# Kernel optimization log

Hardware: AMD Instinct MI355X
Metric: run time of the kernel (lower is better)

## Reference

```python
import jax, jax.numpy as jnp
import numpy as np

# Model dims (match init_kwargs)
D_MODEL = 512
NUM_EXPERTS = 8
TOP_K = 2
FFN_MULT = 2
HIDDEN = FFN_MULT * D_MODEL
BATCH, SEQ = 4, 2048


def setup_inputs() -> dict:
    key = jax.random.key(0)
    k_x, k_g, k_bg, k_w1, k_w3, k_w2 = jax.random.split(key, 6)
    sd = 1.0 / np.sqrt(D_MODEL).astype(np.float32)
    sh = 1.0 / np.sqrt(HIDDEN).astype(np.float32)
    return {
        "x": jax.random.normal(k_x, (BATCH, SEQ, D_MODEL), dtype=jnp.float32),
        # gate: nn.Linear(d_model, num_experts) with bias
        "Wg": jax.random.normal(k_g, (D_MODEL, NUM_EXPERTS), dtype=jnp.float32) * sd,
        "bg": jax.random.normal(k_bg, (NUM_EXPERTS,), dtype=jnp.float32) * 0.01,
        # stacked per-expert SwiGLU FFN params (no bias, LLaMA-style)
        "W1": jax.random.normal(k_w1, (NUM_EXPERTS, D_MODEL, HIDDEN), dtype=jnp.float32) * sd,
        "W3": jax.random.normal(k_w3, (NUM_EXPERTS, D_MODEL, HIDDEN), dtype=jnp.float32) * sd,
        "W2": jax.random.normal(k_w2, (NUM_EXPERTS, HIDDEN, D_MODEL), dtype=jnp.float32) * sh,
    }


def reference(x, Wg, bg, W1, W3, W2):
    B, S, D = x.shape
    E = Wg.shape[1]
    xt = x.reshape(-1, D)                        # [T, D], T = B*S
    T = xt.shape[0]

    # Router: top-k over experts, softmax over the k selected logits
    logits = xt @ Wg + bg                        # [T, E]
    top_vals, top_idx = jax.lax.top_k(logits, TOP_K)  # [T, K]
    top_probs = jax.nn.softmax(top_vals, axis=-1)     # [T, K]

    # Dense per-(token, expert) combine weight; zero where expert not selected.
    # top-k indices are distinct per token so scatter-add == scatter-set.
    gate_w = jnp.zeros((T, E), dtype=xt.dtype).at[
        jnp.arange(T)[:, None], top_idx
    ].add(top_probs)                              # [T, E]

    # Loop over experts (fixed, small), accumulate weighted expert outputs.
    def body(y, expert):
        w1, w3, w2, g = expert                   # g: [T]
        h = jax.nn.silu(xt @ w1) * (xt @ w3)     # [T, H]
        return y + g[:, None] * (h @ w2), None

    y0 = jnp.zeros_like(xt)
    y, _ = jax.lax.scan(body, y0, (W1, W3, W2, gate_w.T))
    return y.reshape(B, S, D)
```

## Files before the change

kernel.cpp:

```cpp
#include <hip/hip_runtime.h>
#include <hip/hip_bf16.h>

#define TOKENS 8192
#define DM 512
#define NE 8
#define HID 1024
#define NSLOT (TOKENS * 2)
#define NB 32

#define BM 128
#define BN 64
#define BK 64
#define BN2 128
#define MAXTILE 136

typedef __bf16 bf16x8 __attribute__((ext_vector_type(8)));
typedef float floatx4 __attribute__((ext_vector_type(4)));
typedef unsigned short u16x8 __attribute__((ext_vector_type(8)));

__device__ __forceinline__ unsigned short f2bf(float f) {
    union { float f; unsigned u; } c; c.f = f;
    unsigned u = c.u;
    u += 0x7fffu + ((u >> 16) & 1u);
    return (unsigned short)(u >> 16);
}

__device__ __forceinline__ void load16_lds(const void* g, void* l) {
    __builtin_amdgcn_global_load_lds(
        (const __attribute__((address_space(1))) unsigned int*)g,
        (__attribute__((address_space(3))) unsigned int*)l, 16, 0, 0);
}

__global__ void cvt_transpose_kernel(const float* __restrict__ W1, const float* __restrict__ W3,
                                     const float* __restrict__ W2,
                                     unsigned short* __restrict__ w1t, unsigned short* __restrict__ w3t,
                                     unsigned short* __restrict__ w2t) {
    __shared__ float tile[64][65];
    const float* src; unsigned short* dst; int K, N;
    if (blockIdx.y == 0)      { src = W1; dst = w1t; K = DM;  N = HID; }
    else if (blockIdx.y == 1) { src = W3; dst = w3t; K = DM;  N = HID; }
    else                      { src = W2; dst = w2t; K = HID; N = DM;  }
    const int tkn = (K >> 6) * (N >> 6);
    int b = blockIdx.x;
    int e = b / tkn;
    int rem = b % tkn;
    const int tn6 = N >> 6;
    int kt = rem / tn6, nt = rem % tn6;
    int tx = threadIdx.x & 15, ty = threadIdx.x >> 4;
    const float* s = src + ((size_t)(e * K + kt * 64 + ty)) * N + nt * 64 + tx * 4;
    #pragma unroll
    for (int i = 0; i < 4; i++) {
        float4 v = *(const float4*)(s + (size_t)(i * 16) * N);
        float* tr = &tile[ty + i * 16][tx * 4];
        tr[0] = v.x; tr[1] = v.y; tr[2] = v.z; tr[3] = v.w;
    }
    __syncthreads();
    int n = threadIdx.x >> 3;
    int c8 = (threadIdx.x & 7) * 8;
    unsigned short* d = dst + ((size_t)(e * N + nt * 64)) * K + kt * 64;
    #pragma unroll
    for (int i = 0; i < 2; i++) {
        int nn = n + i * 32;
        u16x8 r;
        #pragma unroll
        for (int kk = 0; kk < 8; kk++) r[kk] = f2bf(tile[c8 + kk][nn]);
        *(u16x8*)(d + (size_t)nn * K + c8) = r;
    }
}

__global__ void router_kernel(const float* __restrict__ x, const float* __restrict__ Wg,
                              const float* __restrict__ bg,
                              int* __restrict__ top_idx, float* __restrict__ top_p,
                              unsigned short* __restrict__ xb) {
    int lane = threadIdx.x & 63, wave = threadIdx.x >> 6;
    int t = blockIdx.x * 4 + wave;
    float acc[NE];
    #pragma unroll
    for (int e = 0; e < NE; e++) acc[e] = 0.f;
    const float* xr = x + (size_t)t * DM;
    unsigned short* xbr = xb + (size_t)t * DM;
    #pragma unroll
    for (int j = 0; j < 8; j++) {
        int d = lane + j * 64;
        float xv = xr[d];
        xbr[d] = f2bf(xv);
        const float4* wr = (const float4*)(Wg + (size_t)d * NE);
        float4 w0 = wr[0], w1 = wr[1];
        acc[0] += xv * w0.x; acc[1] += xv * w0.y; acc[2] += xv * w0.z; acc[3] += xv * w0.w;
        acc[4] += xv * w1.x; acc[5] += xv * w1.y; acc[6] += xv * w1.z; acc[7] += xv * w1.w;
    }
    #pragma unroll
    for (int e = 0; e < NE; e++) {
        float v = acc[e];
        #pragma unroll
        for (int off = 32; off > 0; off >>= 1) v += __shfl_down(v, off, 64);
        acc[e] = v;
    }
    if (lane == 0) {
        float best = -1e30f, second = -1e30f;
        int bi = 0, si = 0;
        #pragma unroll
        for (int e = 0; e < NE; e++) {
            float v = acc[e] + bg[e];
            if (v > best) { second = best; si = bi; best = v; bi = e; }
            else if (v > second) { second = v; si = e; }
        }
        float ex = __expf(second - best);
        float inv = 1.f / (1.f + ex);
        top_idx[t * 2] = bi;  top_idx[t * 2 + 1] = si;
        top_p[t * 2] = inv;   top_p[t * 2 + 1] = ex * inv;
    }
}

__global__ void hist_kernel(const int* __restrict__ top_idx, int* __restrict__ block_hist) {
    __shared__ int h[NE];
    int b = blockIdx.x, tid = threadIdx.x;
    if (tid < NE) h[tid] = 0;
    __syncthreads();
    int t = b * 256 + tid;
    atomicAdd(&h[top_idx[t * 2]], 1);
    atomicAdd(&h[top_idx[t * 2 + 1]], 1);
    __syncthreads();
    if (tid < NE) block_hist[b * NE + tid] = h[tid];
}

__global__ void prefix_kernel(const int* __restrict__ block_hist, int* __restrict__ counts,
                              int* __restrict__ offsets, int* __restrict__ bases) {
    int e = threadIdx.x;
    if (e < NE) {
        int run = 0;
        for (int b = 0; b < NB; b++) { bases[b * NE + e] = run; run += block_hist[b * NE + e]; }
        counts[e] = run;
    }
    __syncthreads();
    if (e == 0) {
        int s = 0;
        for (int ee = 0; ee < NE; ee++) { offsets[ee] = s; s += counts[ee]; }
    }
    __syncthreads();
    if (e < NE) {
        int off = offsets[e];
        for (int b = 0; b < NB; b++) bases[b * NE + e] += off;
    }
}

__global__ void build_kernel(const int* __restrict__ top_idx, const float* __restrict__ top_p,
                             const int* __restrict__ bases,
                             int* __restrict__ rows, float* __restrict__ gates,
                             int* __restrict__ slot_of) {
    __shared__ int cur[NE];
    int b = blockIdx.x, tid = threadIdx.x;
    if (tid < NE) cur[tid] = bases[b * NE + tid];
    __syncthreads();
    int t = b * 256 + tid;
    #pragma unroll
    for (int k = 0; k < 2; k++) {
        int e = top_idx[t * 2 + k];
        int slot = atomicAdd(&cur[e], 1);
        rows[slot] = t;
        gates[slot] = top_p[t * 2 + k];
        slot_of[t * 2 + k] = slot;
    }
}

__device__ __forceinline__ bool tile_lookup(const int* counts, const int* offsets, int gy,
                                            int& e, int& mt, int& cnt, int& off) {
    int bacc = 0;
    #pragma unroll
    for (int ee = 0; ee < NE; ee++) {
        int c = counts[ee];
        int ntl = (c + BM - 1) >> 7;
        if (gy < bacc + ntl) { e = ee; mt = gy - bacc; cnt = c; off = offsets[ee]; return true; }
        bacc += ntl;
    }
    return false;
}

__global__ __launch_bounds__(256) void gemm1_kernel(
    const unsigned short* __restrict__ xb,
    const unsigned short* __restrict__ w1t,
    const unsigned short* __restrict__ w3t,
    unsigned short* __restrict__ Hb,
    const int* __restrict__ rows, const int* __restrict__ counts,
    const int* __restrict__ offsets) {
    const int lid = blockIdx.x;
    const int xcd = lid & 7;
    const int j = lid >> 3;
    const int gy = xcd * (MAXTILE / 8) + (j >> 4);
    const int nt = j & 15;
    int e, mt, cnt, off;
    if (!tile_lookup(counts, offsets, gy, e, mt, cnt, off)) return;

    __shared__ unsigned short As[BM * BK];
    __shared__ unsigned short B1s[BN * BK];
    __shared__ unsigned short B3s[BN * BK];

    const int tid = threadIdx.x;
    const int lane = tid & 63, wave = tid >> 6;
    const int lrow8 = lane >> 3;
    const int lchunk = (lane & 7) ^ lrow8;

    const unsigned short* a_g[4];
    #pragma unroll
    for (int i = 0; i < 4; i++) {
        int r = (wave * 4 + i) * 8 + lrow8;
        int gr = mt * BM + r;
        int tok = rows[off + (gr < cnt ? gr : 0)];
        a_g[i] = xb + (size_t)tok * DM + lchunk * 8;
    }
    const unsigned short* b1_g[2]; const unsigned short* b3_g[2];
    #pragma unroll
    for (int i = 0; i < 2; i++) {
        int r = (wave * 2 + i) * 8 + lrow8;
        b1_g[i] = w1t + ((size_t)e * HID + nt * BN + r) * DM + lchunk * 8;
        b3_g[i] = w3t + ((size_t)e * HID + nt * BN + r) * DM + lchunk * 8;
    }

    const int l15 = lane & 15, quad = lane >> 4;
    const int sw = l15 & 7;

    floatx4 acc1[2][4], acc3[2][4];
    #pragma unroll
    for (int i = 0; i < 2; i++)
        #pragma unroll
        for (int j2 = 0; j2 < 4; j2++) {
            acc1[i][j2] = (floatx4){0.f, 0.f, 0.f, 0.f};
            acc3[i][j2] = (floatx4){0.f, 0.f, 0.f, 0.f};
        }

    auto stage = [&](int k0) {
        #pragma unroll
        for (int i = 0; i < 4; i++) load16_lds(a_g[i] + k0, &As[(wave * 4 + i) * 512]);
        #pragma unroll
        for (int i = 0; i < 2; i++) {
            load16_lds(b1_g[i] + k0, &B1s[(wave * 2 + i) * 512]);
            load16_lds(b3_g[i] + k0, &B3s[(wave * 2 + i) * 512]);
        }
    };
    auto compute = [&]() {
        #pragma unroll
        for (int kk = 0; kk < 2; kk++) {
            const int qc = kk * 4 + quad;
            const int ch = (qc ^ sw) << 3;
            bf16x8 af[2], b1f[4], b3f[4];
            #pragma unroll
            for (int mi = 0; mi < 2; mi++)
                af[mi] = *(const bf16x8*)(&As[(wave * 32 + mi * 16 + l15) * 64 + ch]);
            #pragma unroll
            for (int ni = 0; ni < 4; ni++) {
                b1f[ni] = *(const bf16x8*)(&B1s[(ni * 16 + l15) * 64 + ch]);
                b3f[ni] = *(const bf16x8*)(&B3s[(ni * 16 + l15) * 64 + ch]);
            }
            #pragma unroll
            for (int mi = 0; mi < 2; mi++)
                #pragma unroll
                for (int ni = 0; ni < 4; ni++) {
                    acc1[mi][ni] = __builtin_amdgcn_mfma_f32_16x16x32_bf16(af[mi], b1f[ni], acc1[mi][ni], 0, 0, 0);
                    acc3[mi][ni] = __builtin_amdgcn_mfma_f32_16x16x32_bf16(af[mi], b3f[ni], acc3[mi][ni], 0, 0, 0);
                }
        }
    };

    const int NI = DM / BK;
    #pragma unroll
    for (int i = 0; i < NI; i++) {
        if (i) __syncthreads();
        stage(i * BK);
        __syncthreads();
        compute();
    }
    #pragma unroll
    for (int mi = 0; mi < 2; mi++) {
        #pragma unroll
        for (int r = 0; r < 4; r++) {
            int mloc = wave * 32 + mi * 16 + quad * 4 + r;
            int gi = mt * BM + mloc;
            if (gi < cnt) {
                size_t rowbase = (size_t)(off + gi) * HID + nt * BN;
                #pragma unroll
                for (int ni = 0; ni < 4; ni++) {
                    float z1 = acc1[mi][ni][r];
                    float z3 = acc3[mi][ni][r];
                    float h = (z1 / (1.f + __expf(-z1))) * z3;
                    Hb[rowbase + ni * 16 + l15] = f2bf(h);
                }
            }
        }
    }
}

__global__ __launch_bounds__(256) void gemm2_kernel(
    const unsigned short* __restrict__ Hb,
    const unsigned short* __restrict__ w2t,
    unsigned short* __restrict__ P,
    const float* __restrict__ gates,
    const int* __restrict__ counts, const int* __restrict__ offsets) {
    const int lid = blockIdx.x;
    const int xcd = lid & 7;
    const int j = lid >> 3;
    const int gy = xcd * (MAXTILE / 8) + (j >> 2);
    const int nt = j & 3;
    int e, mt, cnt, off;
    if (!tile_lookup(counts, offsets, gy, e, mt, cnt, off)) return;

    __shared__ unsigned short As[BM * BK];
    __shared__ unsigned short Bs[BN2 * BK];

    const int tid = threadIdx.x;
    const int lane = tid & 63, wave = tid >> 6;
    const int lrow8 = lane >> 3;
    const int lchunk = (lane & 7) ^ lrow8;

    const unsigned short* a_g[4];
    #pragma unroll
    for (int i = 0; i < 4; i++) {
        int r = (wave * 4 + i) * 8 + lrow8;
        int sl = off + mt * BM + r;
        if (sl >= NSLOT) sl = NSLOT - 1;
        a_g[i] = Hb + (size_t)sl * HID + lchunk * 8;
    }
    const unsigned short* b_g[4];
    #pragma unroll
    for (int i = 0; i < 4; i++) {
        int r = (wave * 4 + i) * 8 + lrow8;
        b_g[i] = w2t + ((size_t)e * DM + nt * BN2 + r) * HID + lchunk * 8;
    }

    const int l15 = lane & 15, quad = lane >> 4;
    const int sw = l15 & 7;

    floatx4 acc[2][8];
    #pragma unroll
    for (int i = 0; i < 2; i++)
        #pragma unroll
        for (int j2 = 0; j2 < 8; j2++) acc[i][j2] = (floatx4){0.f, 0.f, 0.f, 0.f};

    auto stage = [&](int k0) {
        #pragma unroll
        for (int i = 0; i < 4; i++) load16_lds(a_g[i] + k0, &As[(wave * 4 + i) * 512]);
        #pragma unroll
        for (int i = 0; i < 4; i++) load16_lds(b_g[i] + k0, &Bs[(wave * 4 + i) * 512]);
    };
    auto compute = [&]() {
        #pragma unroll
        for (int kk = 0; kk < 2; kk++) {
            const int qc = kk * 4 + quad;
            const int ch = (qc ^ sw) << 3;
            bf16x8 af[2], bf[8];
            #pragma unroll
            for (int mi = 0; mi < 2; mi++)
                af[mi] = *(const bf16x8*)(&As[(wave * 32 + mi * 16 + l15) * 64 + ch]);
            #pragma unroll
            for (int ni = 0; ni < 8; ni++)
                bf[ni] = *(const bf16x8*)(&Bs[(ni * 16 + l15) * 64 + ch]);
            #pragma unroll
            for (int mi = 0; mi < 2; mi++)
                #pragma unroll
                for (int ni = 0; ni < 8; ni++)
                    acc[mi][ni] = __builtin_amdgcn_mfma_f32_16x16x32_bf16(af[mi], bf[ni], acc[mi][ni], 0, 0, 0);
        }
    };

    const int NI = HID / BK;
    #pragma unroll
    for (int i = 0; i < NI; i++) {
        if (i) __syncthreads();
        stage(i * BK);
        __syncthreads();
        compute();
    }
    #pragma unroll
    for (int mi = 0; mi < 2; mi++) {
        #pragma unroll
        for (int r = 0; r < 4; r++) {
            int mloc = wave * 32 + mi * 16 + quad * 4 + r;
            int gi = mt * BM + mloc;
            if (gi < cnt) {
                int slot = off + gi;
                float g = gates[slot];
                #pragma unroll
                for (int ni = 0; ni < 8; ni++) {
                    int col = nt * BN2 + ni * 16 + l15;
                    P[(size_t)slot * DM + col] = f2bf(g * acc[mi][ni][r]);
                }
            }
        }
    }
}

__global__ void combine_kernel(const unsigned short* __restrict__ P,
                               const int* __restrict__ slot_of, float* __restrict__ y) {
    int i = blockIdx.x * blockDim.x + threadIdx.x;
    int t = i / (DM / 8);
    int c8 = i % (DM / 8);
    int s0 = slot_of[t * 2], s1 = slot_of[t * 2 + 1];
    uint4 a = *(const uint4*)(P + (size_t)s0 * DM + c8 * 8);
    uint4 b = *(const uint4*)(P + (size_t)s1 * DM + c8 * 8);
    float o[8];
    const unsigned* aw = (const unsigned*)&a;
    const unsigned* bw = (const unsigned*)&b;
    #pragma unroll
    for (int j = 0; j < 4; j++) {
        union { unsigned u; float f; } al, ah, bl, bh;
        al.u = aw[j] << 16; ah.u = aw[j] & 0xffff0000u;
        bl.u = bw[j] << 16; bh.u = bw[j] & 0xffff0000u;
        o[j * 2]     = al.f + bl.f;
        o[j * 2 + 1] = ah.f + bh.f;
    }
    float4* yo = (float4*)(y + (size_t)t * DM + c8 * 8);
    yo[0] = make_float4(o[0], o[1], o[2], o[3]);
    yo[1] = make_float4(o[4], o[5], o[6], o[7]);
}

extern "C" void kernel_launch(void* const* d_in, const int* in_sizes, int n_in,
                              void* d_out, int out_size, void* d_ws, size_t ws_size,
                              hipStream_t stream) {
    (void)in_sizes; (void)n_in; (void)out_size; (void)ws_size;
    const float* x  = (const float*)d_in[0];
    const float* Wg = (const float*)d_in[1];
    const float* bg = (const float*)d_in[2];
    const float* W1 = (const float*)d_in[3];
    const float* W3 = (const float*)d_in[4];
    const float* W2 = (const float*)d_in[5];
    float* y = (float*)d_out;

    char* p = (char*)d_ws;
    auto carve = [&](size_t bytes) -> char* {
        char* r = p;
        p += (bytes + 255) & ~(size_t)255;
        return r;
    };
    unsigned short* xb   = (unsigned short*)carve((size_t)TOKENS * DM * 2);
    unsigned short* w1t  = (unsigned short*)carve((size_t)NE * DM * HID * 2);
    unsigned short* w3t  = (unsigned short*)carve((size_t)NE * DM * HID * 2);
    unsigned short* w2t  = (unsigned short*)carve((size_t)NE * HID * DM * 2);
    unsigned short* Hb   = (unsigned short*)carve((size_t)NSLOT * HID * 2);
    int*   rows    = (int*)carve(NSLOT * 4);
    float* gates   = (float*)carve(NSLOT * 4);
    int*   slot_of = (int*)carve(NSLOT * 4);
    int*   tidx    = (int*)carve((size_t)TOKENS * 2 * 4);
    float* tp      = (float*)carve((size_t)TOKENS * 2 * 4);
    int*   counts  = (int*)carve(256);
    int*   offsets = (int*)carve(256);
    int*   bhist   = (int*)carve((size_t)NB * NE * 4);
    int*   bases   = (int*)carve((size_t)NB * NE * 4);
    unsigned short* P = w1t;

    router_kernel<<<dim3(TOKENS / 4), dim3(256), 0, stream>>>(x, Wg, bg, tidx, tp, xb);
    cvt_transpose_kernel<<<dim3(NE * 8 * 16, 3), dim3(256), 0, stream>>>(W1, W3, W2, w1t, w3t, w2t);
    hist_kernel<<<dim3(NB), dim3(256), 0, stream>>>(tidx, bhist);
    prefix_kernel<<<dim3(1), dim3(64), 0, stream>>>(bhist, counts, offsets, bases);
    build_kernel<<<dim3(NB), dim3(256), 0, stream>>>(tidx, tp, bases, rows, gates, slot_of);
    gemm1_kernel<<<dim3((HID / BN) * MAXTILE), dim3(256), 0, stream>>>(xb, w1t, w3t, Hb, rows, counts, offsets);
    gemm2_kernel<<<dim3((DM / BN2) * MAXTILE), dim3(256), 0, stream>>>(Hb, w2t, P, gates, counts, offsets);
    combine_kernel<<<dim3((TOKENS * DM / 8) / 256), dim3(256), 0, stream>>>(P, slot_of, y);
}
```

Baseline: 199.5 us.

## Fuse router with weight conversion, split-K gemm2 with atomic scatter into output

Merges the router and weight convert/transpose kernels into one launch. gemm2 now splits the hidden dimension in two and atomically adds gated results straight into y, which removes the bf16 P buffer and the combine kernel. y is zeroed with a memset beforehand. This doubles the gemm2 grid for more parallelism but adds four fp32 atomics per output element (two K halves times two experts) and makes the summation order nondeterministic.

```diff
diff --git a/kernel.cpp b/kernel.cpp
--- a/kernel.cpp
+++ b/kernel.cpp
@@ -31,84 +31,87 @@
         (__attribute__((address_space(3))) unsigned int*)l, 16, 0, 0);
 }
 
-__global__ void cvt_transpose_kernel(const float* __restrict__ W1, const float* __restrict__ W3,
-                                     const float* __restrict__ W2,
-                                     unsigned short* __restrict__ w1t, unsigned short* __restrict__ w3t,
-                                     unsigned short* __restrict__ w2t) {
-    __shared__ float tile[64][65];
-    const float* src; unsigned short* dst; int K, N;
-    if (blockIdx.y == 0)      { src = W1; dst = w1t; K = DM;  N = HID; }
-    else if (blockIdx.y == 1) { src = W3; dst = w3t; K = DM;  N = HID; }
-    else                      { src = W2; dst = w2t; K = HID; N = DM;  }
-    const int tkn = (K >> 6) * (N >> 6);
-    int b = blockIdx.x;
-    int e = b / tkn;
-    int rem = b % tkn;
-    const int tn6 = N >> 6;
-    int kt = rem / tn6, nt = rem % tn6;
-    int tx = threadIdx.x & 15, ty = threadIdx.x >> 4;
-    const float* s = src + ((size_t)(e * K + kt * 64 + ty)) * N + nt * 64 + tx * 4;
-    #pragma unroll
-    for (int i = 0; i < 4; i++) {
-        float4 v = *(const float4*)(s + (size_t)(i * 16) * N);
-        float* tr = &tile[ty + i * 16][tx * 4];
-        tr[0] = v.x; tr[1] = v.y; tr[2] = v.z; tr[3] = v.w;
-    }
-    __syncthreads();
-    int n = threadIdx.x >> 3;
-    int c8 = (threadIdx.x & 7) * 8;
-    unsigned short* d = dst + ((size_t)(e * N + nt * 64)) * K + kt * 64;
-    #pragma unroll
-    for (int i = 0; i < 2; i++) {
-        int nn = n + i * 32;
-        u16x8 r;
-        #pragma unroll
-        for (int kk = 0; kk < 8; kk++) r[kk] = f2bf(tile[c8 + kk][nn]);
-        *(u16x8*)(d + (size_t)nn * K + c8) = r;
-    }
-}
-
-__global__ void router_kernel(const float* __restrict__ x, const float* __restrict__ Wg,
-                              const float* __restrict__ bg,
-                              int* __restrict__ top_idx, float* __restrict__ top_p,
-                              unsigned short* __restrict__ xb) {
-    int lane = threadIdx.x & 63, wave = threadIdx.x >> 6;
-    int t = blockIdx.x * 4 + wave;
-    float acc[NE];
-    #pragma unroll
-    for (int e = 0; e < NE; e++) acc[e] = 0.f;
-    const float* xr = x + (size_t)t * DM;
-    unsigned short* xbr = xb + (size_t)t * DM;
-    #pragma unroll
-    for (int j = 0; j < 8; j++) {
-        int d = lane + j * 64;
-        float xv = xr[d];
-        xbr[d] = f2bf(xv);
-        const float4* wr = (const float4*)(Wg + (size_t)d * NE);
-        float4 w0 = wr[0], w1 = wr[1];
-        acc[0] += xv * w0.x; acc[1] += xv * w0.y; acc[2] += xv * w0.z; acc[3] += xv * w0.w;
-        acc[4] += xv * w1.x; acc[5] += xv * w1.y; acc[6] += xv * w1.z; acc[7] += xv * w1.w;
-    }
-    #pragma unroll
-    for (int e = 0; e < NE; e++) {
-        float v = acc[e];
-        #pragma unroll
-        for (int off = 32; off > 0; off >>= 1) v += __shfl_down(v, off, 64);
-        acc[e] = v;
-    }
-    if (lane == 0) {
-        float best = -1e30f, second = -1e30f;
-        int bi = 0, si = 0;
+__global__ void prep_kernel(const float* __restrict__ x, const float* __restrict__ Wg,
+                            const float* __restrict__ bg,
+                            const float* __restrict__ W1, const float* __restrict__ W3,
+                            const float* __restrict__ W2,
+                            unsigned short* __restrict__ w1t, unsigned short* __restrict__ w3t,
+                            unsigned short* __restrict__ w2t,
+                            int* __restrict__ top_idx, float* __restrict__ top_p,
+                            unsigned short* __restrict__ xb) {
+    if (blockIdx.x < 3072) {
+        __shared__ float tile[64][65];
+        const int cb = blockIdx.x;
+        const int wsel = cb >> 10;
+        const float* src; unsigned short* dst; int K, N;
+        if (wsel == 0)      { src = W1; dst = w1t; K = DM;  N = HID; }
+        else if (wsel == 1) { src = W3; dst = w3t; K = DM;  N = HID; }
+        else                { src = W2; dst = w2t; K = HID; N = DM;  }
+        const int tkn = (K >> 6) * (N >> 6);
+        int b = cb & 1023;
+        int e = b / tkn;
+        int rem = b % tkn;
+        const int tn6 = N >> 6;
+        int kt = rem / tn6, nt = rem % tn6;
+        int tx = threadIdx.x & 15, ty = threadIdx.x >> 4;
+        const float* s = src + ((size_t)(e * K + kt * 64 + ty)) * N + nt * 64 + tx * 4;
+        #pragma unroll
+        for (int i = 0; i < 4; i++) {
+            float4 v = *(const float4*)(s + (size_t)(i * 16) * N);
+            float* tr = &tile[ty + i * 16][tx * 4];
+            tr[0] = v.x; tr[1] = v.y; tr[2] = v.z; tr[3] = v.w;
+        }
+        __syncthreads();
+        int n = threadIdx.x >> 3;
+        int c8 = (threadIdx.x & 7) * 8;
+        unsigned short* d = dst + ((size_t)(e * N + nt * 64)) * K + kt * 64;
+        #pragma unroll
+        for (int i = 0; i < 2; i++) {
+            int nn = n + i * 32;
+            u16x8 r;
+            #pragma unroll
+            for (int kk = 0; kk < 8; kk++) r[kk] = f2bf(tile[c8 + kk][nn]);
+            *(u16x8*)(d + (size_t)nn * K + c8) = r;
+        }
+    } else {
+        int lane = threadIdx.x & 63, wave = threadIdx.x >> 6;
+        int t = (blockIdx.x - 3072) * 4 + wave;
+        float acc[NE];
+        #pragma unroll
+        for (int e = 0; e < NE; e++) acc[e] = 0.f;
+        const float* xr = x + (size_t)t * DM;
+        unsigned short* xbr = xb + (size_t)t * DM;
+        #pragma unroll
+        for (int j = 0; j < 8; j++) {
+            int d = lane + j * 64;
+            float xv = xr[d];
+            xbr[d] = f2bf(xv);
+            const float4* wr = (const float4*)(Wg + (size_t)d * NE);
+            float4 w0 = wr[0], w1 = wr[1];
+            acc[0] += xv * w0.x; acc[1] += xv * w0.y; acc[2] += xv * w0.z; acc[3] += xv * w0.w;
+            acc[4] += xv * w1.x; acc[5] += xv * w1.y; acc[6] += xv * w1.z; acc[7] += xv * w1.w;
+        }
         #pragma unroll
         for (int e = 0; e < NE; e++) {
-            float v = acc[e] + bg[e];
-            if (v > best) { second = best; si = bi; best = v; bi = e; }
-            else if (v > second) { second = v; si = e; }
-        }
-        float ex = __expf(second - best);
-        float inv = 1.f / (1.f + ex);
-        top_idx[t * 2] = bi;  top_idx[t * 2 + 1] = si;
-        top_p[t * 2] = inv;   top_p[t * 2 + 1] = ex * inv;
+            float v = acc[e];
+            #pragma unroll
+            for (int off = 32; off > 0; off >>= 1) v += __shfl_down(v, off, 64);
+            acc[e] = v;
+        }
+        if (lane == 0) {
+            float best = -1e30f, second = -1e30f;
+            int bi = 0, si = 0;
+            #pragma unroll
+            for (int e = 0; e < NE; e++) {
+                float v = acc[e] + bg[e];
+                if (v > best) { second = best; si = bi; best = v; bi = e; }
+                else if (v > second) { second = v; si = e; }
+            }
+            float ex = __expf(second - best);
+            float inv = 1.f / (1.f + ex);
+            top_idx[t * 2] = bi;  top_idx[t * 2 + 1] = si;
+            top_p[t * 2] = inv;   top_p[t * 2 + 1] = ex * inv;
+        }
     }
 }
 
@@ -146,8 +149,7 @@
 
 __global__ void build_kernel(const int* __restrict__ top_idx, const float* __restrict__ top_p,
                              const int* __restrict__ bases,
-                             int* __restrict__ rows, float* __restrict__ gates,
-                             int* __restrict__ slot_of) {
+                             int* __restrict__ rows, float* __restrict__ gates) {
     __shared__ int cur[NE];
     int b = blockIdx.x, tid = threadIdx.x;
     if (tid < NE) cur[tid] = bases[b * NE + tid];
@@ -159,7 +161,6 @@
         int slot = atomicAdd(&cur[e], 1);
         rows[slot] = t;
         gates[slot] = top_p[t * 2 + k];
-        slot_of[t * 2 + k] = slot;
     }
 }
 
@@ -292,13 +293,15 @@
 __global__ __launch_bounds__(256) void gemm2_kernel(
     const unsigned short* __restrict__ Hb,
     const unsigned short* __restrict__ w2t,
-    unsigned short* __restrict__ P,
+    float* __restrict__ y,
     const float* __restrict__ gates,
+    const int* __restrict__ rows,
     const int* __restrict__ counts, const int* __restrict__ offsets) {
     const int lid = blockIdx.x;
     const int xcd = lid & 7;
     const int j = lid >> 3;
-    const int gy = xcd * (MAXTILE / 8) + (j >> 2);
+    const int gy = xcd * (MAXTILE / 8) + (j >> 3);
+    const int kh = (j >> 2) & 1;
     const int nt = j & 3;
     int e, mt, cnt, off;
     if (!tile_lookup(counts, offsets, gy, e, mt, cnt, off)) return;
@@ -310,6 +313,7 @@
     const int lane = tid & 63, wave = tid >> 6;
     const int lrow8 = lane >> 3;
     const int lchunk = (lane & 7) ^ lrow8;
+    const int kbase = kh * (HID / 2);
 
     const unsigned short* a_g[4];
     #pragma unroll
@@ -317,13 +321,13 @@
         int r = (wave * 4 + i) * 8 + lrow8;
         int sl = off + mt * BM + r;
         if (sl >= NSLOT) sl = NSLOT - 1;
-        a_g[i] = Hb + (size_t)sl * HID + lchunk * 8;
+        a_g[i] = Hb + (size_t)sl * HID + kbase + lchunk * 8;
     }
     const unsigned short* b_g[4];
     #pragma unroll
     for (int i = 0; i < 4; i++) {
         int r = (wave * 4 + i) * 8 + lrow8;
-        b_g[i] = w2t + ((size_t)e * DM + nt * BN2 + r) * HID + lchunk * 8;
+        b_g[i] = w2t + ((size_t)e * DM + nt * BN2 + r) * HID + kbase + lchunk * 8;
     }
 
     const int l15 = lane & 15, quad = lane >> 4;
@@ -361,7 +365,7 @@
         }
     };
 
-    const int NI = HID / BK;
+    const int NI = (HID / 2) / BK;
     #pragma unroll
     for (int i = 0; i < NI; i++) {
         if (i) __syncthreads();
@@ -377,39 +381,16 @@
             int gi = mt * BM + mloc;
             if (gi < cnt) {
                 int slot = off + gi;
+                int tok = rows[slot];
                 float g = gates[slot];
                 #pragma unroll
                 for (int ni = 0; ni < 8; ni++) {
                     int col = nt * BN2 + ni * 16 + l15;
-                    P[(size_t)slot * DM + col] = f2bf(g * acc[mi][ni][r]);
+                    atomicAdd(&y[(size_t)tok * DM + col], g * acc[mi][ni][r]);
                 }
             }
         }
     }
-}
-
-__global__ void combine_kernel(const unsigned short* __restrict__ P,
-                               const int* __restrict__ slot_of, float* __restrict__ y) {
-    int i = blockIdx.x * blockDim.x + threadIdx.x;
-    int t = i / (DM / 8);
-    int c8 = i % (DM / 8);
-    int s0 = slot_of[t * 2], s1 = slot_of[t * 2 + 1];
-    uint4 a = *(const uint4*)(P + (size_t)s0 * DM + c8 * 8);
-    uint4 b = *(const uint4*)(P + (size_t)s1 * DM + c8 * 8);
-    float o[8];
-    const unsigned* aw = (const unsigned*)&a;
-    const unsigned* bw = (const unsigned*)&b;
-    #pragma unroll
-    for (int j = 0; j < 4; j++) {
-        union { unsigned u; float f; } al, ah, bl, bh;
-        al.u = aw[j] << 16; ah.u = aw[j] & 0xffff0000u;
-        bl.u = bw[j] << 16; bh.u = bw[j] & 0xffff0000u;
-        o[j * 2]     = al.f + bl.f;
-        o[j * 2 + 1] = ah.f + bh.f;
-    }
-    float4* yo = (float4*)(y + (size_t)t * DM + c8 * 8);
-    yo[0] = make_float4(o[0], o[1], o[2], o[3]);
-    yo[1] = make_float4(o[4], o[5], o[6], o[7]);
 }
 
 extern "C" void kernel_launch(void* const* d_in, const int* in_sizes, int n_in,
@@ -437,21 +418,19 @@
     unsigned short* Hb   = (unsigned short*)carve((size_t)NSLOT * HID * 2);
     int*   rows    = (int*)carve(NSLOT * 4);
     float* gates   = (float*)carve(NSLOT * 4);
-    int*   slot_of = (int*)carve(NSLOT * 4);
     int*   tidx    = (int*)carve((size_t)TOKENS * 2 * 4);
     float* tp      = (float*)carve((size_t)TOKENS * 2 * 4);
     int*   counts  = (int*)carve(256);
     int*   offsets = (int*)carve(256);
     int*   bhist   = (int*)carve((size_t)NB * NE * 4);
     int*   bases   = (int*)carve((size_t)NB * NE * 4);
-    unsigned short* P = w1t;
-
-    router_kernel<<<dim3(TOKENS / 4), dim3(256), 0, stream>>>(x, Wg, bg, tidx, tp, xb);
-    cvt_transpose_kernel<<<dim3(NE * 8 * 16, 3), dim3(256), 0, stream>>>(W1, W3, W2, w1t, w3t, w2t);
+
+    hipMemsetAsync(y, 0, (size_t)TOKENS * DM * sizeof(float), stream);
+    prep_kernel<<<dim3(3072 + TOKENS / 4), dim3(256), 0, stream>>>(
+        x, Wg, bg, W1, W3, W2, w1t, w3t, w2t, tidx, tp, xb);
     hist_kernel<<<dim3(NB), dim3(256), 0, stream>>>(tidx, bhist);
     prefix_kernel<<<dim3(1), dim3(64), 0, stream>>>(bhist, counts, offsets, bases);
-    build_kernel<<<dim3(NB), dim3(256), 0, stream>>>(tidx, tp, bases, rows, gates, slot_of);
+    build_kernel<<<dim3(NB), dim3(256), 0, stream>>>(tidx, tp, bases, rows, gates);
     gemm1_kernel<<<dim3((HID / BN) * MAXTILE), dim3(256), 0, stream>>>(xb, w1t, w3t, Hb, rows, counts, offsets);
-    gemm2_kernel<<<dim3((DM / BN2) * MAXTILE), dim3(256), 0, stream>>>(Hb, w2t, P, gates, counts, offsets);
-    combine_kernel<<<dim3((TOKENS * DM / 8) / 256), dim3(256), 0, stream>>>(P, slot_of, y);
-}
+    gemm2_kernel<<<dim3(8 * MAXTILE), dim3(256), 0, stream>>>(Hb, w2t, y, gates, rows, counts, offsets);
+}
```

New measurement: 230.4 us. +15.5%, slower.
